# Optimization experiments

Hardware: AMD Instinct MI355X
Metric: run time of the kernel (lower is better)

The kernel has to match this reference:

```python
import jax, jax.numpy as jnp
import numpy as np

OUT_DIM = 4096
NCROPS = 10
STUDENT_TEMP = 0.1
WARMUP_TEACHER_TEMP = 0.04
TEACHER_TEMP = 0.07
WARMUP_EPOCHS = 30
NEPOCHS = 100
B = 32
NG = 196
NL = 36
DFEAT = 384


def _l2norm(x, eps=1e-12):
    n = jnp.sqrt(jnp.sum(x * x, axis=-1, keepdims=True))
    return x / jnp.maximum(n, eps)


def setup_inputs() -> dict:
    key = jax.random.key(0)
    ks = jax.random.split(key, 6)
    s_rows = B * (2 * NG + (NCROPS - 2) * NL)  # 21760
    t_rows = 2 * B * NG  # 12544
    return {
        "student_cls_pred": jax.random.normal(ks[0], (NCROPS * B, OUT_DIM), jnp.float32),
        "student_region_pred": jax.random.normal(ks[1], (s_rows, OUT_DIM), jnp.float32),
        "student_feats": jax.random.normal(ks[2], (s_rows, DFEAT), jnp.float32),
        "teacher_cls_pred": jax.random.normal(ks[3], (2 * B, OUT_DIM), jnp.float32),
        "teacher_region_pred": jax.random.normal(ks[4], (t_rows, OUT_DIM), jnp.float32),
        "teacher_feats": jax.random.normal(ks[5], (t_rows, DFEAT), jnp.float32),
        "center": jnp.zeros((1, OUT_DIM), jnp.float32),
        "center_grid": jnp.zeros((1, OUT_DIM), jnp.float32),
        "epoch": 50,
        "n_global": 196,
        "n_local": 36,
    }


def reference(student_cls_pred, student_region_pred, student_feats,
              teacher_cls_pred, teacher_region_pred, teacher_feats,
              center, center_grid, epoch, n_global, n_local):
    sched = np.concatenate((np.linspace(WARMUP_TEACHER_TEMP, TEACHER_TEMP, WARMUP_EPOCHS),
                            np.ones(NEPOCHS - WARMUP_EPOCHS) * TEACHER_TEMP))
    temp = float(sched[epoch])

    b = teacher_cls_pred.shape[0] // 2
    N = n_global

    # teacher targets (detached in torch)
    t_cls = jax.lax.stop_gradient(jax.nn.softmax((teacher_cls_pred - center) / temp, axis=-1))
    t_reg = jax.lax.stop_gradient(jax.nn.softmax((teacher_region_pred - center_grid) / temp, axis=-1))
    t_cls_chunks = jnp.split(t_cls, 2, axis=0)
    t_reg_chunks = jnp.split(t_reg, 2, axis=0)
    t_fea_chunks = jnp.split(teacher_feats, 2, axis=0)

    s_cls = student_cls_pred / STUDENT_TEMP
    s_cls_chunks = jnp.split(s_cls, NCROPS, axis=0)

    split_sizes = [n_global] * 2 + [n_local] * (NCROPS - 2)
    offsets = np.cumsum([0] + [s * b for s in split_sizes])
    s_reg_scaled = student_region_pred / STUDENT_TEMP
    s_reg_chunks = [s_reg_scaled[offsets[k]:offsets[k + 1]] for k in range(NCROPS)]
    s_fea_chunks = [student_feats[offsets[k]:offsets[k + 1]] for k in range(NCROPS)]

    total_loss = jnp.zeros((), student_cls_pred.dtype)
    n_terms = 0
    for i in range(2):
        q = t_cls_chunks[i]                                   # [b, D]
        t_region = t_reg_chunks[i].reshape(b, N, -1)          # [b, N, D]
        t_fea = _l2norm(t_fea_chunks[i].reshape(b, N, -1))    # [b, N, F]
        for j in range(NCROPS):
            if j == i:
                continue
            v = s_cls_chunks[j]
            loss = 0.5 * jnp.sum(-q * jax.nn.log_softmax(v, axis=-1), axis=-1)  # [b]

            S = split_sizes[j]
            s_region = s_reg_chunks[j].reshape(b, S, -1)      # [b, S, D]
            s_fea = _l2norm(s_fea_chunks[j].reshape(b, S, -1))
            sim = jnp.einsum('bsf,bnf->bsn', s_fea, t_fea)    # cosine sim [b, S, N]
            ind = jnp.argmax(sim, axis=2)                     # [b, S]
            t_indexed = jnp.take_along_axis(t_region, ind[:, :, None], axis=1)  # [b, S, D]
            loss = loss + 0.5 * jnp.mean(
                jnp.sum(-t_indexed * jax.nn.log_softmax(s_region, axis=-1), axis=-1), axis=-1)
            total_loss = total_loss + jnp.mean(loss)
            n_terms += 1
    return total_loss / n_terms
```

## Files before the change

kernel.cpp:

```cpp
#include <hip/hip_runtime.h>
#include <math.h>

#define D 4096
#define F 384
#define NB 32
#define NG 196
#define NL 36
#define SROWS 21760
#define TROWS 12544
#define TCHUNK 6272
#define LCHUNK 1152
#define NPART (SROWS + 576)

__device__ inline float get_invtemp(const int* ep_ptr) {
  int ep = *ep_ptr;
  double t = (ep < 30) ? (0.04 + (double)ep * (0.03 / 29.0)) : 0.07;
  return 1.0f / (float)t;
}

__device__ inline float warp_max(float v) {
#pragma unroll
  for (int o = 32; o; o >>= 1) v = fmaxf(v, __shfl_xor(v, o));
  return v;
}
__device__ inline float warp_sum(float v) {
#pragma unroll
  for (int o = 32; o; o >>= 1) v += __shfl_xor(v, o);
  return v;
}
__device__ inline float block_max(float v, float* sc) {
  v = warp_max(v);
  __syncthreads();
  if ((threadIdx.x & 63) == 0) sc[threadIdx.x >> 6] = v;
  __syncthreads();
  return fmaxf(fmaxf(sc[0], sc[1]), fmaxf(sc[2], sc[3]));
}
__device__ inline float block_sum(float v, float* sc) {
  v = warp_sum(v);
  __syncthreads();
  if ((threadIdx.x & 63) == 0) sc[threadIdx.x >> 6] = v;
  __syncthreads();
  return (sc[0] + sc[1]) + (sc[2] + sc[3]);
}

__device__ inline unsigned long long umax64(unsigned long long a, unsigned long long b) {
  return a > b ? a : b;
}
__device__ inline unsigned long long pack_key(float sim, int tc) {
  unsigned bts = __float_as_uint(sim);
  bts = (bts & 0x80000000u) ? ~bts : (bts | 0x80000000u);
  return ((unsigned long long)bts << 32) | (unsigned long long)(0xFFFFFFFFu - (unsigned)tc);
}
__device__ inline void unpack4(float4 v, float* dst) {
  dst[0] = v.x; dst[1] = v.y; dst[2] = v.z; dst[3] = v.w;
}

__global__ __launch_bounds__(256) void k_tnorm(const float* __restrict__ tfea,
                                               float* __restrict__ invtn) {
  int gw = (blockIdx.x * 256 + threadIdx.x) >> 6;
  int lane = threadIdx.x & 63;
  if (gw >= TROWS) return;
  const float* p = tfea + (size_t)gw * F;
  float ss = 0.f;
#pragma unroll
  for (int k = 0; k < 6; k++) { float v = p[lane + 64 * k]; ss += v * v; }
  ss = warp_sum(ss);
  if (lane == 0) invtn[gw] = 1.0f / fmaxf(sqrtf(ss), 1e-12f);
}

__global__ __launch_bounds__(256) void k_sim(const float* __restrict__ sfea,
                                             const float* __restrict__ tfea,
                                             const float* __restrict__ invtn,
                                             unsigned long long* __restrict__ keys) {
  __shared__ float s_sm[64][65];
  __shared__ float t_sm0[64][65];
  __shared__ float t_sm1[64][65];
  int tid = threadIdx.x;
  int bid = blockIdx.x;
  int st = bid >> 2, tt = bid & 3;
  int b = st >> 4, w = st & 15;
  int j, tile;
  if (w < 4)      { j = 0; tile = w; }
  else if (w < 8) { j = 1; tile = w - 4; }
  else            { j = 2 + (w - 8); tile = 0; }
  int S = (j < 2) ? NG : NL;
  int off = (j < 2) ? j * TCHUNK : 2 * TCHUNK + (j - 2) * LCHUNK;
  int base_s = off + b * S + tile * 64;
  int vs = S - tile * 64; if (vs > 64) vs = 64;
  bool ni2 = (j >= 2);
  int i0 = (j == 0) ? 1 : 0;
  int tc0 = tt * 64;
  int vt = NG - tc0; if (vt > 64) vt = 64;
  int trb0 = i0 * TCHUNK + b * NG + tc0;
  int trb1 = TCHUNK + b * NG + tc0;
  int tx = tid & 15, ty = tid >> 4;

  float acc0[4][4] = {{0.f}}, acc1[4][4] = {{0.f}};

  for (int kt = 0; kt < 6; kt++) {
    int k0 = kt * 64;
    __syncthreads();
#pragma unroll
    for (int rr = 0; rr < 4; rr++) {
      int idx = rr * 256 + tid;
      int row = idx >> 4, c4 = idx & 15;
      float4 v = make_float4(0.f, 0.f, 0.f, 0.f);
      if (row < vs) v = *(const float4*)(sfea + (size_t)(base_s + row) * F + k0 + c4 * 4);
      s_sm[row][c4 * 4 + 0] = v.x; s_sm[row][c4 * 4 + 1] = v.y;
      s_sm[row][c4 * 4 + 2] = v.z; s_sm[row][c4 * 4 + 3] = v.w;
    }
#pragma unroll
    for (int rr = 0; rr < 4; rr++) {
      int idx = rr * 256 + tid;
      int row = idx >> 4, c4 = idx & 15;
      float4 v = make_float4(0.f, 0.f, 0.f, 0.f);
      if (row < vt) v = *(const float4*)(tfea + (size_t)(trb0 + row) * F + k0 + c4 * 4);
      t_sm0[row][c4 * 4 + 0] = v.x; t_sm0[row][c4 * 4 + 1] = v.y;
      t_sm0[row][c4 * 4 + 2] = v.z; t_sm0[row][c4 * 4 + 3] = v.w;
    }
    if (ni2) {
#pragma unroll
      for (int rr = 0; rr < 4; rr++) {
        int idx = rr * 256 + tid;
        int row = idx >> 4, c4 = idx & 15;
        float4 v = make_float4(0.f, 0.f, 0.f, 0.f);
        if (row < vt) v = *(const float4*)(tfea + (size_t)(trb1 + row) * F + k0 + c4 * 4);
        t_sm1[row][c4 * 4 + 0] = v.x; t_sm1[row][c4 * 4 + 1] = v.y;
        t_sm1[row][c4 * 4 + 2] = v.z; t_sm1[row][c4 * 4 + 3] = v.w;
      }
    }
    __syncthreads();
#pragma unroll 8
    for (int kk = 0; kk < 64; kk++) {
      float sv[4], tv[4];
#pragma unroll
      for (int m = 0; m < 4; m++) sv[m] = s_sm[ty * 4 + m][kk];
#pragma unroll
      for (int n = 0; n < 4; n++) tv[n] = t_sm0[tx * 4 + n][kk];
#pragma unroll
      for (int m = 0; m < 4; m++)
#pragma unroll
        for (int n = 0; n < 4; n++) acc0[m][n] += sv[m] * tv[n];
      if (ni2) {
        float wv[4];
#pragma unroll
        for (int n = 0; n < 4; n++) wv[n] = t_sm1[tx * 4 + n][kk];
#pragma unroll
        for (int m = 0; m < 4; m++)
#pragma unroll
          for (int n = 0; n < 4; n++) acc1[m][n] += sv[m] * wv[n];
      }
    }
  }

  float inv0[4], inv1[4];
#pragma unroll
  for (int n = 0; n < 4; n++) {
    int tc = tx * 4 + n;
    inv0[n] = (tc < vt) ? invtn[trb0 + tc] : 0.f;
    inv1[n] = (ni2 && tc < vt) ? invtn[trb1 + tc] : 0.f;
  }
#pragma unroll
  for (int m = 0; m < 4; m++) {
    int sl = ty * 4 + m;
    unsigned long long best0 = 0ull, best1 = 0ull;
#pragma unroll
    for (int n = 0; n < 4; n++) {
      int tcl = tx * 4 + n;
      if (tcl < vt) {
        int tc = tc0 + tcl;
        best0 = umax64(best0, pack_key(acc0[m][n] * inv0[n], tc));
        if (ni2) best1 = umax64(best1, pack_key(acc1[m][n] * inv1[n], tc));
      }
    }
#pragma unroll
    for (int o = 1; o < 16; o <<= 1) {
      best0 = umax64(best0, __shfl_xor(best0, o));
      best1 = umax64(best1, __shfl_xor(best1, o));
    }
    if (tx == 0 && sl < vs) {
      atomicMax(&keys[(size_t)i0 * SROWS + base_s + sl], best0);
      if (ni2) atomicMax(&keys[(size_t)SROWS + base_s + sl], best1);
    }
  }
}

__global__ __launch_bounds__(256) void k_region(const float* __restrict__ sreg,
                                                const float* __restrict__ treg,
                                                const float* __restrict__ cgrid,
                                                const unsigned long long* __restrict__ keys,
                                                const int* __restrict__ epoch,
                                                float* __restrict__ partials) {
  __shared__ float sc[4];
  int r = blockIdx.x, tid = threadIdx.x;
  int j, rem;
  if (r < TCHUNK)          { j = 0; rem = r; }
  else if (r < 2 * TCHUNK) { j = 1; rem = r - TCHUNK; }
  else { int q = r - 2 * TCHUNK; j = 2 + q / LCHUNK; rem = q - (j - 2) * LCHUNK; }
  int S = (j < 2) ? NG : NL;
  int b = rem / S;
  float invtemp = get_invtemp(epoch);

  const float4* sp = (const float4*)(sreg + (size_t)r * D);
  float sv[16];
  unpack4(sp[tid], sv); unpack4(sp[tid + 256], sv + 4);
  unpack4(sp[tid + 512], sv + 8); unpack4(sp[tid + 768], sv + 12);
#pragma unroll
  for (int k = 0; k < 16; k++) sv[k] *= 10.f;

  float m = -INFINITY;
#pragma unroll
  for (int k = 0; k < 16; k++) m = fmaxf(m, sv[k]);
  float M = block_max(m, sc);
  float e = 0.f;
#pragma unroll
  for (int k = 0; k < 16; k++) e += expf(sv[k] - M);
  float Ssum = block_sum(e, sc);
  float base = M + logf(Ssum);

  const float4* cp = (const float4*)cgrid;
  float cv[16];
  unpack4(cp[tid], cv); unpack4(cp[tid + 256], cv + 4);
  unpack4(cp[tid + 512], cv + 8); unpack4(cp[tid + 768], cv + 12);

  int ni = (j >= 2) ? 2 : 1;
  int i0 = (j == 0) ? 1 : 0;
  float wsel = 0.5f / (float)(S * NB * 18);
  float acc = 0.f;
  for (int q = 0; q < ni; q++) {
    int i = (q == 0) ? i0 : 1;
    unsigned long long kv = keys[(size_t)i * SROWS + r];
    int ind = (int)(0xFFFFFFFFu - (unsigned)(kv & 0xFFFFFFFFull));
    const float4* tp = (const float4*)(treg + (size_t)(i * TCHUNK + b * NG + ind) * D);
    float tv[16];
    unpack4(tp[tid], tv); unpack4(tp[tid + 256], tv + 4);
    unpack4(tp[tid + 512], tv + 8); unpack4(tp[tid + 768], tv + 12);
#pragma unroll
    for (int k = 0; k < 16; k++) tv[k] = (tv[k] - cv[k]) * invtemp;
    float tm = -INFINITY;
#pragma unroll
    for (int k = 0; k < 16; k++) tm = fmaxf(tm, tv[k]);
    float Tm = block_max(tm, sc);
    float es = 0.f, ed = 0.f;
#pragma unroll
    for (int k = 0; k < 16; k++) {
      float ee = expf(tv[k] - Tm);
      es += ee; ed += ee * sv[k];
    }
    es = block_sum(es, sc);
    ed = block_sum(ed, sc);
    acc += wsel * (base - ed / es);
  }
  if (tid == 0) partials[r] = acc;
}

__global__ __launch_bounds__(256) void k_cls(const float* __restrict__ scls,
                                             const float* __restrict__ tcls,
                                             const float* __restrict__ center,
                                             const int* __restrict__ epoch,
                                             float* __restrict__ part) {
  __shared__ float sc[4];
  int bid = blockIdx.x, tid = threadIdx.x;
  int p = bid >> 5, b = bid & 31;
  int i = p / 9, jj = p % 9;
  int j = (jj < i) ? jj : jj + 1;
  float invtemp = get_invtemp(epoch);

  const float4* sp = (const float4*)(scls + (size_t)(j * NB + b) * D);
  float sv[16];
  unpack4(sp[tid], sv); unpack4(sp[tid + 256], sv + 4);
  unpack4(sp[tid + 512], sv + 8); unpack4(sp[tid + 768], sv + 12);
#pragma unroll
  for (int k = 0; k < 16; k++) sv[k] *= 10.f;
  float m = -INFINITY;
#pragma unroll
  for (int k = 0; k < 16; k++) m = fmaxf(m, sv[k]);
  float M = block_max(m, sc);
  float e = 0.f;
#pragma unroll
  for (int k = 0; k < 16; k++) e += expf(sv[k] - M);
  float Ssum = block_sum(e, sc);
  float base = M + logf(Ssum);

  const float4* cp = (const float4*)center;
  const float4* tp = (const float4*)(tcls + (size_t)(i * NB + b) * D);
  float tv[16], cv[16];
  unpack4(cp[tid], cv); unpack4(cp[tid + 256], cv + 4);
  unpack4(cp[tid + 512], cv + 8); unpack4(cp[tid + 768], cv + 12);
  unpack4(tp[tid], tv); unpack4(tp[tid + 256], tv + 4);
  unpack4(tp[tid + 512], tv + 8); unpack4(tp[tid + 768], tv + 12);
#pragma unroll
  for (int k = 0; k < 16; k++) tv[k] = (tv[k] - cv[k]) * invtemp;
  float tm = -INFINITY;
#pragma unroll
  for (int k = 0; k < 16; k++) tm = fmaxf(tm, tv[k]);
  float Tm = block_max(tm, sc);
  float es = 0.f, ed = 0.f;
#pragma unroll
  for (int k = 0; k < 16; k++) {
    float ee = expf(tv[k] - Tm);
    es += ee; ed += ee * sv[k];
  }
  es = block_sum(es, sc);
  ed = block_sum(ed, sc);
  if (tid == 0) part[bid] = (base - ed / es) * (0.5f / 576.f);
}

__global__ __launch_bounds__(1024) void k_final(const float* __restrict__ partials,
                                                float* __restrict__ out, int n) {
  __shared__ float sc[16];
  int tid = threadIdx.x;
  float s = 0.f;
  for (int idx = tid; idx < n; idx += 1024) s += partials[idx];
  s = warp_sum(s);
  if ((tid & 63) == 0) sc[tid >> 6] = s;
  __syncthreads();
  if (tid < 64) {
    float v = (tid < 16) ? sc[tid] : 0.f;
    v = warp_sum(v);
    if (tid == 0) out[0] = v;
  }
}

extern "C" void kernel_launch(void* const* d_in, const int* in_sizes, int n_in,
                              void* d_out, int out_size, void* d_ws, size_t ws_size,
                              hipStream_t stream) {
  const float* s_cls = (const float*)d_in[0];
  const float* s_reg = (const float*)d_in[1];
  const float* s_fea = (const float*)d_in[2];
  const float* t_cls = (const float*)d_in[3];
  const float* t_reg = (const float*)d_in[4];
  const float* t_fea = (const float*)d_in[5];
  const float* center = (const float*)d_in[6];
  const float* cgrid = (const float*)d_in[7];
  const int* epoch = (const int*)d_in[8];

  char* ws = (char*)d_ws;
  unsigned long long* keys = (unsigned long long*)ws;
  float* invtn = (float*)(ws + 348160);
  float* partials = (float*)(ws + 398336);

  hipMemsetAsync(keys, 0, (size_t)2 * SROWS * sizeof(unsigned long long), stream);
  k_tnorm<<<TROWS / 4, 256, 0, stream>>>(t_fea, invtn);
  k_sim<<<2048, 256, 0, stream>>>(s_fea, t_fea, invtn, keys);
  k_region<<<SROWS, 256, 0, stream>>>(s_reg, t_reg, cgrid, keys, epoch, partials);
  k_cls<<<576, 256, 0, stream>>>(s_cls, t_cls, center, epoch, partials + SROWS);
  k_final<<<1, 1024, 0, stream>>>(partials, (float*)d_out, NPART);
}
```

Before: 931.3 us.

## Restructure similarity GEMM: k-major shared tiles, packed local crops, register prefetch

The cosine-similarity kernel now packs the eight local crops of a batch into one 288-row student tile space. This cuts the block count from 2048 to 1664 and removes the mostly idle 36-of-64 row tiles. Shared tiles are stored k-major with K=32 so the inner loop can use float4 LDS reads. Global loads are issued into registers before the barrier, and the two-teacher and one-teacher paths get separate specialized loops. The cost is a little more index arithmetic to map packed rows back to real rows, plus twice as many k-iterations.

```diff
diff --git a/kernel.cpp b/kernel.cpp
--- a/kernel.cpp
+++ b/kernel.cpp
@@ -11,6 +11,8 @@
 #define TCHUNK 6272
 #define LCHUNK 1152
 #define NPART (SROWS + 576)
+#define KT 32
+#define PADW 68
 
 __device__ inline float get_invtemp(const int* ep_ptr) {
   int ep = *ep_ptr;
@@ -53,6 +55,14 @@
 }
 __device__ inline void unpack4(float4 v, float* dst) {
   dst[0] = v.x; dst[1] = v.y; dst[2] = v.z; dst[3] = v.w;
+}
+
+__device__ inline int srow_of(int cat, int b, int p) {
+  if (cat == 0) return b * NG + p;
+  if (cat == 1) return TCHUNK + b * NG + p;
+  int j = p / 36;
+  int pos = p - j * 36;
+  return 2 * TCHUNK + j * LCHUNK + b * NL + pos;
 }
 
 __global__ __launch_bounds__(256) void k_tnorm(const float* __restrict__ tfea,
@@ -72,115 +82,130 @@
                                              const float* __restrict__ tfea,
                                              const float* __restrict__ invtn,
                                              unsigned long long* __restrict__ keys) {
-  __shared__ float s_sm[64][65];
-  __shared__ float t_sm0[64][65];
-  __shared__ float t_sm1[64][65];
+  __shared__ float s_km[KT][PADW];
+  __shared__ float tA_km[KT][PADW];
+  __shared__ float tB_km[KT][PADW];
   int tid = threadIdx.x;
   int bid = blockIdx.x;
-  int st = bid >> 2, tt = bid & 3;
-  int b = st >> 4, w = st & 15;
-  int j, tile;
-  if (w < 4)      { j = 0; tile = w; }
-  else if (w < 8) { j = 1; tile = w - 4; }
-  else            { j = 2 + (w - 8); tile = 0; }
-  int S = (j < 2) ? NG : NL;
-  int off = (j < 2) ? j * TCHUNK : 2 * TCHUNK + (j - 2) * LCHUNK;
-  int base_s = off + b * S + tile * 64;
-  int vs = S - tile * 64; if (vs > 64) vs = 64;
-  bool ni2 = (j >= 2);
-  int i0 = (j == 0) ? 1 : 0;
+  int tt = bid & 3;
+  int rest = bid >> 2;
+  int st = rest % 13;
+  int b = rest / 13;
+  int cat, base_p;
+  if (st < 4)      { cat = 0; base_p = st * 64; }
+  else if (st < 8) { cat = 1; base_p = (st - 4) * 64; }
+  else             { cat = 2; base_p = (st - 8) * 64; }
+  int vs = ((cat < 2) ? NG : 288) - base_p; if (vs > 64) vs = 64;
+  bool ni2 = (cat == 2);
+  int iA = (cat == 0) ? 1 : 0;
   int tc0 = tt * 64;
   int vt = NG - tc0; if (vt > 64) vt = 64;
-  int trb0 = i0 * TCHUNK + b * NG + tc0;
-  int trb1 = TCHUNK + b * NG + tc0;
+  int gA = iA * TCHUNK + b * NG + tc0;
+  int gB = TCHUNK + b * NG + tc0;
   int tx = tid & 15, ty = tid >> 4;
 
-  float acc0[4][4] = {{0.f}}, acc1[4][4] = {{0.f}};
-
-  for (int kt = 0; kt < 6; kt++) {
-    int k0 = kt * 64;
+  int row0 = tid >> 3, c4 = tid & 7;
+  int row1 = row0 + 32;
+  bool sv0 = row0 < vs, sv1 = row1 < vs;
+  bool tv0 = row0 < vt, tv1 = row1 < vt;
+  const float* sp0 = sfea + (size_t)srow_of(cat, b, base_p + (sv0 ? row0 : 0)) * F + c4 * 4;
+  const float* sp1 = sfea + (size_t)srow_of(cat, b, base_p + (sv1 ? row1 : 0)) * F + c4 * 4;
+  const float* tpA0 = tfea + (size_t)(gA + (tv0 ? row0 : 0)) * F + c4 * 4;
+  const float* tpA1 = tfea + (size_t)(gA + (tv1 ? row1 : 0)) * F + c4 * 4;
+  const float* tpB0 = tfea + (size_t)(gB + (tv0 ? row0 : 0)) * F + c4 * 4;
+  const float* tpB1 = tfea + (size_t)(gB + (tv1 ? row1 : 0)) * F + c4 * 4;
+  int kbase = c4 * 4;
+
+  float accA[4][4] = {{0.f}}, accB[4][4] = {{0.f}};
+  const float4 z4 = make_float4(0.f, 0.f, 0.f, 0.f);
+
+  for (int kt = 0; kt < F / KT; kt++) {
+    int k0 = kt * KT;
+    float4 a0 = sv0 ? *(const float4*)(sp0 + k0) : z4;
+    float4 a1 = sv1 ? *(const float4*)(sp1 + k0) : z4;
+    float4 b0 = tv0 ? *(const float4*)(tpA0 + k0) : z4;
+    float4 b1 = tv1 ? *(const float4*)(tpA1 + k0) : z4;
+    float4 c0 = z4, c1 = z4;
+    if (ni2) {
+      c0 = tv0 ? *(const float4*)(tpB0 + k0) : z4;
+      c1 = tv1 ? *(const float4*)(tpB1 + k0) : z4;
+    }
     __syncthreads();
-#pragma unroll
-    for (int rr = 0; rr < 4; rr++) {
-      int idx = rr * 256 + tid;
-      int row = idx >> 4, c4 = idx & 15;
-      float4 v = make_float4(0.f, 0.f, 0.f, 0.f);
-      if (row < vs) v = *(const float4*)(sfea + (size_t)(base_s + row) * F + k0 + c4 * 4);
-      s_sm[row][c4 * 4 + 0] = v.x; s_sm[row][c4 * 4 + 1] = v.y;
-      s_sm[row][c4 * 4 + 2] = v.z; s_sm[row][c4 * 4 + 3] = v.w;
-    }
-#pragma unroll
-    for (int rr = 0; rr < 4; rr++) {
-      int idx = rr * 256 + tid;
-      int row = idx >> 4, c4 = idx & 15;
-      float4 v = make_float4(0.f, 0.f, 0.f, 0.f);
-      if (row < vt) v = *(const float4*)(tfea + (size_t)(trb0 + row) * F + k0 + c4 * 4);
-      t_sm0[row][c4 * 4 + 0] = v.x; t_sm0[row][c4 * 4 + 1] = v.y;
-      t_sm0[row][c4 * 4 + 2] = v.z; t_sm0[row][c4 * 4 + 3] = v.w;
-    }
+    s_km[kbase + 0][row0] = a0.x; s_km[kbase + 1][row0] = a0.y;
+    s_km[kbase + 2][row0] = a0.z; s_km[kbase + 3][row0] = a0.w;
+    s_km[kbase + 0][row1] = a1.x; s_km[kbase + 1][row1] = a1.y;
+    s_km[kbase + 2][row1] = a1.z; s_km[kbase + 3][row1] = a1.w;
+    tA_km[kbase + 0][row0] = b0.x; tA_km[kbase + 1][row0] = b0.y;
+    tA_km[kbase + 2][row0] = b0.z; tA_km[kbase + 3][row0] = b0.w;
+    tA_km[kbase + 0][row1] = b1.x; tA_km[kbase + 1][row1] = b1.y;
+    tA_km[kbase + 2][row1] = b1.z; tA_km[kbase + 3][row1] = b1.w;
     if (ni2) {
-#pragma unroll
-      for (int rr = 0; rr < 4; rr++) {
-        int idx = rr * 256 + tid;
-        int row = idx >> 4, c4 = idx & 15;
-        float4 v = make_float4(0.f, 0.f, 0.f, 0.f);
-        if (row < vt) v = *(const float4*)(tfea + (size_t)(trb1 + row) * F + k0 + c4 * 4);
-        t_sm1[row][c4 * 4 + 0] = v.x; t_sm1[row][c4 * 4 + 1] = v.y;
-        t_sm1[row][c4 * 4 + 2] = v.z; t_sm1[row][c4 * 4 + 3] = v.w;
+      tB_km[kbase + 0][row0] = c0.x; tB_km[kbase + 1][row0] = c0.y;
+      tB_km[kbase + 2][row0] = c0.z; tB_km[kbase + 3][row0] = c0.w;
+      tB_km[kbase + 0][row1] = c1.x; tB_km[kbase + 1][row1] = c1.y;
+      tB_km[kbase + 2][row1] = c1.z; tB_km[kbase + 3][row1] = c1.w;
+    }
+    __syncthreads();
+    if (ni2) {
+#pragma unroll 8
+      for (int kk = 0; kk < KT; kk++) {
+        float4 s4 = *(const float4*)&s_km[kk][ty * 4];
+        float4 t4 = *(const float4*)&tA_km[kk][tx * 4];
+        float4 u4 = *(const float4*)&tB_km[kk][tx * 4];
+        float sv[4], tv[4], uv[4];
+        unpack4(s4, sv); unpack4(t4, tv); unpack4(u4, uv);
+#pragma unroll
+        for (int m = 0; m < 4; m++)
+#pragma unroll
+          for (int n = 0; n < 4; n++) {
+            accA[m][n] += sv[m] * tv[n];
+            accB[m][n] += sv[m] * uv[n];
+          }
       }
-    }
-    __syncthreads();
+    } else {
 #pragma unroll 8
-    for (int kk = 0; kk < 64; kk++) {
-      float sv[4], tv[4];
-#pragma unroll
-      for (int m = 0; m < 4; m++) sv[m] = s_sm[ty * 4 + m][kk];
-#pragma unroll
-      for (int n = 0; n < 4; n++) tv[n] = t_sm0[tx * 4 + n][kk];
-#pragma unroll
-      for (int m = 0; m < 4; m++)
-#pragma unroll
-        for (int n = 0; n < 4; n++) acc0[m][n] += sv[m] * tv[n];
-      if (ni2) {
-        float wv[4];
-#pragma unroll
-        for (int n = 0; n < 4; n++) wv[n] = t_sm1[tx * 4 + n][kk];
+      for (int kk = 0; kk < KT; kk++) {
+        float4 s4 = *(const float4*)&s_km[kk][ty * 4];
+        float4 t4 = *(const float4*)&tA_km[kk][tx * 4];
+        float sv[4], tv[4];
+        unpack4(s4, sv); unpack4(t4, tv);
 #pragma unroll
         for (int m = 0; m < 4; m++)
 #pragma unroll
-          for (int n = 0; n < 4; n++) acc1[m][n] += sv[m] * wv[n];
+          for (int n = 0; n < 4; n++) accA[m][n] += sv[m] * tv[n];
       }
     }
   }
 
-  float inv0[4], inv1[4];
+  float invA[4], invB[4];
 #pragma unroll
   for (int n = 0; n < 4; n++) {
-    int tc = tx * 4 + n;
-    inv0[n] = (tc < vt) ? invtn[trb0 + tc] : 0.f;
-    inv1[n] = (ni2 && tc < vt) ? invtn[trb1 + tc] : 0.f;
+    int tcl = tx * 4 + n;
+    invA[n] = (tcl < vt) ? invtn[gA + tcl] : 0.f;
+    invB[n] = (ni2 && tcl < vt) ? invtn[gB + tcl] : 0.f;
   }
 #pragma unroll
   for (int m = 0; m < 4; m++) {
     int sl = ty * 4 + m;
-    unsigned long long best0 = 0ull, best1 = 0ull;
+    unsigned long long bestA = 0ull, bestB = 0ull;
 #pragma unroll
     for (int n = 0; n < 4; n++) {
       int tcl = tx * 4 + n;
       if (tcl < vt) {
         int tc = tc0 + tcl;
-        best0 = umax64(best0, pack_key(acc0[m][n] * inv0[n], tc));
-        if (ni2) best1 = umax64(best1, pack_key(acc1[m][n] * inv1[n], tc));
+        bestA = umax64(bestA, pack_key(accA[m][n] * invA[n], tc));
+        if (ni2) bestB = umax64(bestB, pack_key(accB[m][n] * invB[n], tc));
       }
     }
 #pragma unroll
     for (int o = 1; o < 16; o <<= 1) {
-      best0 = umax64(best0, __shfl_xor(best0, o));
-      best1 = umax64(best1, __shfl_xor(best1, o));
+      bestA = umax64(bestA, __shfl_xor(bestA, o));
+      bestB = umax64(bestB, __shfl_xor(bestB, o));
     }
     if (tx == 0 && sl < vs) {
-      atomicMax(&keys[(size_t)i0 * SROWS + base_s + sl], best0);
-      if (ni2) atomicMax(&keys[(size_t)SROWS + base_s + sl], best1);
+      int sr = srow_of(cat, b, base_p + sl);
+      atomicMax(&keys[(size_t)iA * SROWS + sr], bestA);
+      if (ni2) atomicMax(&keys[(size_t)SROWS + sr], bestB);
     }
   }
 }
@@ -342,7 +367,7 @@
 
   hipMemsetAsync(keys, 0, (size_t)2 * SROWS * sizeof(unsigned long long), stream);
   k_tnorm<<<TROWS / 4, 256, 0, stream>>>(t_fea, invtn);
-  k_sim<<<2048, 256, 0, stream>>>(s_fea, t_fea, invtn, keys);
+  k_sim<<<32 * 13 * 4, 256, 0, stream>>>(s_fea, t_fea, invtn, keys);
   k_region<<<SROWS, 256, 0, stream>>>(s_reg, t_reg, cgrid, keys, epoch, partials);
   k_cls<<<576, 256, 0, stream>>>(s_cls, t_cls, center, epoch, partials + SROWS);
   k_final<<<1, 1024, 0, stream>>>(partials, (float*)d_out, NPART);
```

Result: faster. 795.6 us (-14.6%).
